# Kernel tuning notes

Measured on AMD Instinct MI355X. Metric: run time of the kernel, lower is better.

Reference implementation:

```python
import jax, jax.numpy as jnp
import numpy as np

K = 4  # knn_graph(k=4, loop=False) hard-coded in H2GCN.forward


def _knn_2hop_adj(Fet, k):
    """Per-batch kNN graph -> symmetrize -> 2-hop binary adjacency [B,N,N].

    Matches create_adj + get_2hop_neighbors: edge direction and the row
    normalization in create_adj are irrelevant because get_2hop_neighbors
    symmetrizes (adj[row,col]=adj[col,row]=1) and thresholds (adj@adj > 0).
    """
    B, N, _ = Fet.shape
    sq = jnp.sum(Fet * Fet, axis=-1)  # [B,N]
    dist = sq[:, :, None] + sq[:, None, :] - 2.0 * jnp.einsum('bnf,bmf->bnm', Fet, Fet)
    eye = jnp.eye(N, dtype=bool)
    dist = jnp.where(eye[None], jnp.inf, dist)  # loop=False: exclude self
    _, idx = jax.lax.top_k(-dist, k)  # [B,N,k] nearest-neighbor indices
    b_idx = jnp.arange(B)[:, None, None]
    n_idx = jnp.arange(N)[None, :, None]
    A = jnp.zeros((B, N, N), Fet.dtype).at[b_idx, n_idx, idx].set(1.0)
    A = jnp.maximum(A, jnp.swapaxes(A, 1, 2))  # symmetrize 1-hop
    A2 = jnp.einsum('bnm,bmk->bnk', A, A)      # 2-hop counts
    A2 = jnp.where(eye[None], 0.0, A2)          # fill_diagonal_(0)
    return (A2 > 0).astype(Fet.dtype)


def _h2gcn_conv(x, A2, w1, b1, w2, b2):
    """H2GCNConv on dense binary adjacency.

    Dense matmul with binary A2 == gather(x[col]) -> fc2 -> index_add over rows;
    A2.sum(-1) == bincount(row). Degree clamped to >= 1.
    """
    ego = jnp.einsum('bnf,of->bno', x, w1) + b1   # fc1(x)
    msg = jnp.einsum('bnf,of->bno', x, w2) + b2   # fc2(x)
    agg = jnp.einsum('bnm,bmo->bno', A2, msg)     # scatter-add of neighbor msgs
    deg = jnp.maximum(jnp.sum(A2, axis=-1, keepdims=True), 1.0)
    return jax.nn.relu(jnp.concatenate([ego, agg / deg], axis=-1))


def setup_inputs() -> dict:
    key = jax.random.key(0)
    ks = jax.random.split(key, 8)
    B, N, F, NH, NC = 128, 197, 768, 512, 1000
    s = 0.02
    return {
        'Fet': jax.random.normal(ks[0], (B, N, F), jnp.float32),
        'w1_0': jax.random.normal(ks[1], (NH, F), jnp.float32) * s,
        'b1_0': jnp.zeros((NH,), jnp.float32),
        'w2_0': jax.random.normal(ks[2], (NH, F), jnp.float32) * s,
        'b2_0': jnp.zeros((NH,), jnp.float32),
        'w1_1': jax.random.normal(ks[3], (NH, 2 * NH), jnp.float32) * s,
        'b1_1': jnp.zeros((NH,), jnp.float32),
        'w2_1': jax.random.normal(ks[4], (NH, 2 * NH), jnp.float32) * s,
        'b2_1': jnp.zeros((NH,), jnp.float32),
        'fc1_w': jax.random.normal(ks[5], (NH, 4 * NH), jnp.float32) * s,
        'fc1_b': jnp.zeros((NH,), jnp.float32),
        'fc2_w': jax.random.normal(ks[6], (NC, NH), jnp.float32) * s,
        'fc2_b': jnp.zeros((NC,), jnp.float32),
    }


def reference(Fet, w1_0, b1_0, w2_0, b2_0, w1_1, b1_1, w2_1, b2_1,
              fc1_w, fc1_b, fc2_w, fc2_b):
    A2 = _knn_2hop_adj(Fet, K)
    h1 = _h2gcn_conv(Fet, A2, w1_0, b1_0, w2_0, b2_0)   # [B,N,2*nhid]
    h2 = _h2gcn_conv(h1, A2, w1_1, b1_1, w2_1, b2_1)    # [B,N,2*nhid]
    h = jnp.concatenate([h1, h2], axis=-1)              # [B,N,final_dim]
    graph_features = jnp.mean(h, axis=1)                # global_mean_pool
    p = jax.nn.relu(graph_features @ fc1_w.T + fc1_b)   # dropout is identity (eval)
    out = p @ fc2_w.T + fc2_b
    return (out, graph_features)
```

## Files before the change

kernel.cpp:

```cpp
#include <hip/hip_runtime.h>
#include <hip/hip_bf16.h>
#include <math.h>

typedef __attribute__((ext_vector_type(8))) short bf16x8;
typedef __attribute__((ext_vector_type(4))) float f32x4;

#define B_ 128
#define N_ 197
#define F_ 768
#define NH_ 512
#define D2_ 1024
#define D4_ 2048
#define NC_ 1000
#define ROWS_ (B_ * N_)
#define KA_ 224
#define NA_ 256

#define OFF_DIST   0ull
#define OFF_SQ     19871232ull
#define OFF_ABITS  19972352ull
#define OFF_DEG    20779520ull
#define OFF_FETHI  20880640ull
#define OFF_MSG    59710720ull
#define OFF_H1     85564672ull
#define OFF_FETLO  OFF_MSG
#define OFF_POOL   137338112ull
#define OFF_P      138386688ull
#define OFF_W10    138648832ull
#define OFF_W20    139435264ull
#define OFF_W11    140221696ull
#define OFF_W21    141270272ull

__device__ __forceinline__ void gll16(const void* g, void* l) {
  __builtin_amdgcn_global_load_lds((const __attribute__((address_space(1))) void*)g,
                                   (__attribute__((address_space(3))) void*)l, 16, 0, 0);
}

__global__ __launch_bounds__(256) void cast_bf16_kernel(const float* __restrict__ src,
                                                        __hip_bfloat16* __restrict__ dst,
                                                        int n4) {
  int i = blockIdx.x * 256 + threadIdx.x;
  if (i >= n4) return;
  float4 v = ((const float4*)src)[i];
  union { __hip_bfloat16 h[4]; uint2 u; } pk;
  pk.h[0] = __float2bfloat16(v.x);
  pk.h[1] = __float2bfloat16(v.y);
  pk.h[2] = __float2bfloat16(v.z);
  pk.h[3] = __float2bfloat16(v.w);
  ((uint2*)dst)[i] = pk.u;
}

__global__ __launch_bounds__(256) void cast_hilo_kernel(const float* __restrict__ src,
                                                        __hip_bfloat16* __restrict__ hi,
                                                        __hip_bfloat16* __restrict__ lo,
                                                        int n4) {
  int i = blockIdx.x * 256 + threadIdx.x;
  if (i >= n4) return;
  float4 v = ((const float4*)src)[i];
  float f[4] = {v.x, v.y, v.z, v.w};
  union { __hip_bfloat16 h[4]; uint2 u; } ph, pl;
#pragma unroll
  for (int k = 0; k < 4; k++) {
    __hip_bfloat16 h = __float2bfloat16(f[k]);
    ph.h[k] = h;
    pl.h[k] = __float2bfloat16(f[k] - __bfloat162float(h));
  }
  ((uint2*)hi)[i] = ph.u;
  ((uint2*)lo)[i] = pl.u;
}

__global__ __launch_bounds__(256) void sqnorm_kernel(const float* __restrict__ X,
                                                     float* __restrict__ sq) {
  int row = blockIdx.x * 4 + (threadIdx.x >> 6);
  int lane = threadIdx.x & 63;
  const float4* xp = (const float4*)(X + (size_t)row * F_);
  float s = 0.f;
#pragma unroll
  for (int i = 0; i < 3; i++) {
    float4 v = xp[lane + i * 64];
    s += v.x * v.x + v.y * v.y + v.z * v.z + v.w * v.w;
  }
#pragma unroll
  for (int o = 32; o > 0; o >>= 1) s += __shfl_down(s, o);
  if (lane == 0) sq[row] = s;
}

__global__ __launch_bounds__(256) void mfma_gram(const __hip_bfloat16* __restrict__ Xhi,
                                                 const __hip_bfloat16* __restrict__ Xlo,
                                                 const float* __restrict__ sq,
                                                 float* __restrict__ dist) {
  __shared__ short AsH[4096];
  __shared__ short BsH[4096];
  __shared__ short AsL[4096];
  __shared__ short BsL[4096];
  const int t = threadIdx.x;
  const int b = blockIdx.z;
  const int bx = blockIdx.x;
  const int m0 = (bx == 0) ? 0 : 128;
  const int o0 = (bx == 2) ? 128 : 0;
  const bool mirror = (bx == 1);
  const int l = t & 63, w = t >> 6;
  const int wm = (w >> 1) * 64, wn = (w & 1) * 64;
  const int frow = l & 15, fch = l >> 4;
  const int srow = t >> 2, sslot = t & 3;
  const size_t rowbase = (size_t)b * N_;
  const char* AhiB = (const char*)(Xhi + (rowbase + m0) * F_);
  const char* AloB = (const char*)(Xlo + (rowbase + m0) * F_);
  const char* BhiB = (const char*)(Xhi + (rowbase + o0) * F_);
  const char* BloB = (const char*)(Xlo + (rowbase + o0) * F_);
  const int rb = F_ * 2;
  char* AsHB = (char*)AsH;
  char* BsHB = (char*)BsH;
  char* AsLB = (char*)AsL;
  char* BsLB = (char*)BsL;
  f32x4 zero = {0.f, 0.f, 0.f, 0.f};
  f32x4 acc[4][4];
#pragma unroll
  for (int i = 0; i < 4; i++)
#pragma unroll
    for (int j = 0; j < 4; j++) acc[i][j] = zero;
  for (int kt = 0; kt < F_ / 32; kt++) {
    const int kb = kt * 64;
#pragma unroll
    for (int u = 0; u < 2; u++) {
      int grow = u * 64 + srow;
      int gslot = sslot ^ (grow & 3);
      size_t go = (size_t)grow * rb + kb + gslot * 16;
      gll16(AhiB + go, AsHB + u * 4096 + t * 16);
      gll16(BhiB + go, BsHB + u * 4096 + t * 16);
      gll16(AloB + go, AsLB + u * 4096 + t * 16);
      gll16(BloB + go, BsLB + u * 4096 + t * 16);
    }
    __syncthreads();
    bf16x8 ah[4], al[4], bh[4], bl[4];
#pragma unroll
    for (int i = 0; i < 4; i++) {
      int ar = wm + i * 16 + frow;
      int aoff = ar * 64 + ((fch ^ (ar & 3)) * 16);
      ah[i] = *(const bf16x8*)(AsHB + aoff);
      al[i] = *(const bf16x8*)(AsLB + aoff);
      int br = wn + i * 16 + frow;
      int boff = br * 64 + ((fch ^ (br & 3)) * 16);
      bh[i] = *(const bf16x8*)(BsHB + boff);
      bl[i] = *(const bf16x8*)(BsLB + boff);
    }
#pragma unroll
    for (int i = 0; i < 4; i++)
#pragma unroll
      for (int j = 0; j < 4; j++) {
        acc[i][j] = __builtin_amdgcn_mfma_f32_16x16x32_bf16(ah[i], bh[j], acc[i][j], 0, 0, 0);
        acc[i][j] = __builtin_amdgcn_mfma_f32_16x16x32_bf16(ah[i], bl[j], acc[i][j], 0, 0, 0);
        acc[i][j] = __builtin_amdgcn_mfma_f32_16x16x32_bf16(al[i], bh[j], acc[i][j], 0, 0, 0);
      }
    __syncthreads();
  }
#pragma unroll
  for (int j = 0; j < 4; j++) {
    int m = o0 + wn + j * 16 + frow;
    if (m >= N_) continue;
    float sm = sq[rowbase + m];
#pragma unroll
    for (int i = 0; i < 4; i++) {
      int nb = m0 + wm + i * 16 + fch * 4;
#pragma unroll
      for (int r = 0; r < 4; r++) {
        int n = nb + r;
        if (n >= N_) continue;
        float d = sq[rowbase + n] + sm - 2.f * acc[i][j][r];
        if (n == m) d = INFINITY;
        dist[(rowbase + n) * N_ + m] = d;
        if (mirror) dist[(rowbase + m) * N_ + n] = d;
      }
    }
  }
}

__global__ __launch_bounds__(256) void topk_kernel(const float* __restrict__ dist,
                                                   unsigned long long* __restrict__ Abits) {
  int row = blockIdx.x * 4 + (threadIdx.x >> 6);
  int lane = threadIdx.x & 63;
  int b = row / N_, n = row - b * N_;
  const float* dr = dist + (size_t)row * N_;
  float v[4];
  int vi[4];
#pragma unroll
  for (int i = 0; i < 4; i++) {
    int m = lane + i * 64;
    bool ok = (m < N_);
    v[i] = ok ? dr[m] : INFINITY;
    vi[i] = ok ? m : 0x3fffffff;
  }
  unsigned long long nbr[4] = {0ull, 0ull, 0ull, 0ull};
#pragma unroll
  for (int t = 0; t < 4; t++) {
    float bv = v[0];
    int bi = vi[0];
#pragma unroll
    for (int i = 1; i < 4; i++)
      if (v[i] < bv || (v[i] == bv && vi[i] < bi)) { bv = v[i]; bi = vi[i]; }
#pragma unroll
    for (int o = 1; o < 64; o <<= 1) {
      float ov = __shfl_xor(bv, o);
      int oi = __shfl_xor(bi, o);
      if (ov < bv || (ov == bv && oi < bi)) { bv = ov; bi = oi; }
    }
#pragma unroll
    for (int i = 0; i < 4; i++)
      if (vi[i] == bi) { v[i] = INFINITY; vi[i] = 0x3fffffff; }
    if (lane == 0) {
      nbr[bi >> 6] |= 1ull << (bi & 63);
      atomicOr(&Abits[((size_t)b * N_ + bi) * 4 + (n >> 6)], 1ull << (n & 63));
    }
  }
  if (lane == 0) {
#pragma unroll
    for (int w = 0; w < 4; w++)
      if (nbr[w]) atomicOr(&Abits[(size_t)row * 4 + w], nbr[w]);
  }
}

__global__ __launch_bounds__(256) void a2_kernel(const unsigned long long* __restrict__ Abits,
                                                 __hip_bfloat16* __restrict__ A2bf,
                                                 float* __restrict__ deg) {
  int row = blockIdx.x * 4 + (threadIdx.x >> 6);
  int lane = threadIdx.x & 63;
  int b = row / N_, n = row - b * N_;
  const unsigned long long* arow = Abits + (size_t)row * 4;
  const unsigned long long* base = Abits + (size_t)b * N_ * 4;
  unsigned long long r0 = 0, r1 = 0, r2 = 0, r3 = 0;
#pragma unroll
  for (int w = 0; w < 4; w++) {
    if ((arow[w] >> lane) & 1ull) {
      const unsigned long long* mr = base + (size_t)(w * 64 + lane) * 4;
      r0 |= mr[0]; r1 |= mr[1]; r2 |= mr[2]; r3 |= mr[3];
    }
  }
#pragma unroll
  for (int o = 1; o < 64; o <<= 1) {
    r0 |= __shfl_xor(r0, o);
    r1 |= __shfl_xor(r1, o);
    r2 |= __shfl_xor(r2, o);
    r3 |= __shfl_xor(r3, o);
  }
  unsigned long long rr[4] = {r0, r1, r2, r3};
  rr[n >> 6] &= ~(1ull << (n & 63));
  __hip_bfloat16* out = A2bf + ((size_t)b * NA_ + n) * KA_;
  const __hip_bfloat16 one = __float2bfloat16(1.f);
  const __hip_bfloat16 zer = __float2bfloat16(0.f);
#pragma unroll
  for (int i = 0; i < 4; i++) {
    int m = lane + i * 64;
    if (m < KA_)
      out[m] = (m < N_ && ((rr[m >> 6] >> (m & 63)) & 1ull)) ? one : zer;
  }
  if (lane == 0) {
    int dg = __popcll(rr[0]) + __popcll(rr[1]) + __popcll(rr[2]) + __popcll(rr[3]);
    deg[row] = (float)(dg > 0 ? dg : 1);
  }
}

template <bool RELU>
__global__ __launch_bounds__(256) void mfma_linear(const __hip_bfloat16* __restrict__ X,
                                                   const __hip_bfloat16* __restrict__ W,
                                                   const float* __restrict__ bias,
                                                   __hip_bfloat16* __restrict__ Y,
                                                   int K, int ldy, int colOff) {
  __shared__ short As[4096];
  __shared__ short Bs[4096];
  const int t = threadIdx.x;
  const int m0 = blockIdx.y * 128, o0 = blockIdx.x * 128;
  const int l = t & 63, w = t >> 6;
  const int wm = (w >> 1) * 64, wn = (w & 1) * 64;
  const int frow = l & 15, fch = l >> 4;
  const int srow = t >> 2, sslot = t & 3;
  const char* Abase = (const char*)(X + (size_t)m0 * K);
  const char* Bbase = (const char*)(W + (size_t)o0 * K);
  const int rb = K * 2;
  char* AsB = (char*)As;
  char* BsB = (char*)Bs;
  f32x4 zero = {0.f, 0.f, 0.f, 0.f};
  f32x4 acc[4][4];
#pragma unroll
  for (int i = 0; i < 4; i++)
#pragma unroll
    for (int j = 0; j < 4; j++) acc[i][j] = zero;
  const int KT = K >> 5;
  for (int kt = 0; kt < KT; kt++) {
    const int kb = kt * 64;
#pragma unroll
    for (int u = 0; u < 2; u++) {
      int grow = u * 64 + srow;
      int gslot = sslot ^ (grow & 3);
      gll16(Abase + (size_t)grow * rb + kb + gslot * 16, AsB + u * 4096 + t * 16);
      gll16(Bbase + (size_t)grow * rb + kb + gslot * 16, BsB + u * 4096 + t * 16);
    }
    __syncthreads();
    bf16x8 af[4], bfv[4];
#pragma unroll
    for (int i = 0; i < 4; i++) {
      int ar = wm + i * 16 + frow;
      af[i] = *(const bf16x8*)(AsB + ar * 64 + ((fch ^ (ar & 3)) * 16));
      int br = wn + i * 16 + frow;
      bfv[i] = *(const bf16x8*)(BsB + br * 64 + ((fch ^ (br & 3)) * 16));
    }
#pragma unroll
    for (int i = 0; i < 4; i++)
#pragma unroll
      for (int j = 0; j < 4; j++)
        acc[i][j] = __builtin_amdgcn_mfma_f32_16x16x32_bf16(af[i], bfv[j], acc[i][j], 0, 0, 0);
    __syncthreads();
  }
#pragma unroll
  for (int j = 0; j < 4; j++) {
    int c = o0 + wn + j * 16 + frow;
    float bv = bias[c];
#pragma unroll
    for (int i = 0; i < 4; i++) {
      int r0 = m0 + wm + i * 16 + fch * 4;
#pragma unroll
      for (int r = 0; r < 4; r++) {
        float v = acc[i][j][r] + bv;
        if (RELU) v = fmaxf(v, 0.f);
        Y[(size_t)(r0 + r) * ldy + colOff + c] = __float2bfloat16(v);
      }
    }
  }
}

__global__ __launch_bounds__(256) void mfma_ego_pool(const __hip_bfloat16* __restrict__ h1,
                                                     const __hip_bfloat16* __restrict__ W,
                                                     const float* __restrict__ bias,
                                                     float* __restrict__ pool, int poolOff) {
  __shared__ short As[4096];
  __shared__ short Bs[4096];
  const int t = threadIdx.x;
  const int b = blockIdx.z;
  const int m0 = blockIdx.y * 128, o0 = blockIdx.x * 128;
  const int l = t & 63, w = t >> 6;
  const int wm = (w >> 1) * 64, wn = (w & 1) * 64;
  const int frow = l & 15, fch = l >> 4;
  const int srow = t >> 2, sslot = t & 3;
  const char* Abase = (const char*)(h1 + ((size_t)b * N_ + m0) * D2_);
  const char* Bbase = (const char*)(W + (size_t)o0 * D2_);
  char* AsB = (char*)As;
  char* BsB = (char*)Bs;
  f32x4 zero = {0.f, 0.f, 0.f, 0.f};
  f32x4 acc[4][4];
#pragma unroll
  for (int i = 0; i < 4; i++)
#pragma unroll
    for (int j = 0; j < 4; j++) acc[i][j] = zero;
  for (int kt = 0; kt < 32; kt++) {
    const int kb = kt * 64;
#pragma unroll
    for (int u = 0; u < 2; u++) {
      int grow = u * 64 + srow;
      int gslot = sslot ^ (grow & 3);
      gll16(Abase + (size_t)grow * (D2_ * 2) + kb + gslot * 16, AsB + u * 4096 + t * 16);
      gll16(Bbase + (size_t)grow * (D2_ * 2) + kb + gslot * 16, BsB + u * 4096 + t * 16);
    }
    __syncthreads();
    bf16x8 af[4], bfv[4];
#pragma unroll
    for (int i = 0; i < 4; i++) {
      int ar = wm + i * 16 + frow;
      af[i] = *(const bf16x8*)(AsB + ar * 64 + ((fch ^ (ar & 3)) * 16));
      int br = wn + i * 16 + frow;
      bfv[i] = *(const bf16x8*)(BsB + br * 64 + ((fch ^ (br & 3)) * 16));
    }
#pragma unroll
    for (int i = 0; i < 4; i++)
#pragma unroll
      for (int j = 0; j < 4; j++)
        acc[i][j] = __builtin_amdgcn_mfma_f32_16x16x32_bf16(af[i], bfv[j], acc[i][j], 0, 0, 0);
    __syncthreads();
  }
#pragma unroll
  for (int j = 0; j < 4; j++) {
    int c = o0 + wn + j * 16 + frow;
    float bv = bias[c];
    float s = 0.f;
#pragma unroll
    for (int i = 0; i < 4; i++) {
#pragma unroll
      for (int r = 0; r < 4; r++) {
        int n = m0 + wm + i * 16 + fch * 4 + r;
        if (n < N_) s += fmaxf(acc[i][j][r] + bv, 0.f);
      }
    }
    s += __shfl_down(s, 32);
    s += __shfl_down(s, 16);
    if (l < 16) atomicAdd(&pool[(size_t)b * D4_ + poolOff + c], s);
  }
}

template <int MODE>
__global__ __launch_bounds__(256) void mfma_agg(const __hip_bfloat16* __restrict__ A2bf,
                                                const __hip_bfloat16* __restrict__ msg,
                                                const float* __restrict__ deg,
                                                __hip_bfloat16* __restrict__ H,
                                                float* __restrict__ pool, int poolOff) {
  __shared__ short As[4096];
  __shared__ short Bs[4096];
  const int t = threadIdx.x;
  const int b = blockIdx.z;
  const int m0 = blockIdx.y * 128, o0 = blockIdx.x * 128;
  const int l = t & 63, w = t >> 6;
  const int wm = (w >> 1) * 64, wn = (w & 1) * 64;
  const int frow = l & 15, fch = l >> 4;
  const int srow = t >> 2, sslot = t & 3;
  const char* Abase = (const char*)(A2bf + ((size_t)b * NA_ + m0) * KA_);
  const __hip_bfloat16* Mb = msg + (size_t)b * N_ * NH_;
  const int bk = t >> 3;
  const int bf0 = (t & 7) * 16;
  char* AsB = (char*)As;
  char* BsB = (char*)Bs;
  f32x4 zero = {0.f, 0.f, 0.f, 0.f};
  f32x4 acc[4][4];
#pragma unroll
  for (int i = 0; i < 4; i++)
#pragma unroll
    for (int j = 0; j < 4; j++) acc[i][j] = zero;
  for (int kt = 0; kt < 7; kt++) {
#pragma unroll
    for (int u = 0; u < 2; u++) {
      int grow = u * 64 + srow;
      int gslot = sslot ^ (grow & 3);
      gll16(Abase + (size_t)grow * (KA_ * 2) + kt * 64 + gslot * 16, AsB + u * 4096 + t * 16);
    }
    int krow = kt * 32 + bk;
    const __hip_bfloat16* mp = Mb + (size_t)krow * NH_ + o0 + bf0;
    bf16x8 v0 = *(const bf16x8*)mp;
    bf16x8 v1 = *(const bf16x8*)(mp + 8);
#pragma unroll
    for (int e = 0; e < 8; e++) {
      int f0a = bf0 + e;
      int f1a = bf0 + 8 + e;
      *(short*)(BsB + f0a * 64 + (((bk >> 3) ^ (f0a & 3)) * 16) + (bk & 7) * 2) = v0[e];
      *(short*)(BsB + f1a * 64 + (((bk >> 3) ^ (f1a & 3)) * 16) + (bk & 7) * 2) = v1[e];
    }
    __syncthreads();
    bf16x8 af[4], bfv[4];
#pragma unroll
    for (int i = 0; i < 4; i++) {
      int ar = wm + i * 16 + frow;
      af[i] = *(const bf16x8*)(AsB + ar * 64 + ((fch ^ (ar & 3)) * 16));
      int br = wn + i * 16 + frow;
      bfv[i] = *(const bf16x8*)(BsB + br * 64 + ((fch ^ (br & 3)) * 16));
    }
#pragma unroll
    for (int i = 0; i < 4; i++)
#pragma unroll
      for (int j = 0; j < 4; j++)
        acc[i][j] = __builtin_amdgcn_mfma_f32_16x16x32_bf16(af[i], bfv[j], acc[i][j], 0, 0, 0);
    __syncthreads();
  }
  if (MODE == 0) {
#pragma unroll
    for (int j = 0; j < 4; j++) {
      int c = o0 + wn + j * 16 + frow;
#pragma unroll
      for (int i = 0; i < 4; i++) {
#pragma unroll
        for (int r = 0; r < 4; r++) {
          int n = m0 + wm + i * 16 + fch * 4 + r;
          if (n < N_) {
            float dv = deg[b * N_ + n];
            float v = fmaxf(acc[i][j][r] / dv, 0.f);
            H[((size_t)b * N_ + n) * D2_ + NH_ + c] = __float2bfloat16(v);
          }
        }
      }
    }
  } else {
#pragma unroll
    for (int j = 0; j < 4; j++) {
      int c = o0 + wn + j * 16 + frow;
      float s = 0.f;
#pragma unroll
      for (int i = 0; i < 4; i++) {
#pragma unroll
        for (int r = 0; r < 4; r++) {
          int n = m0 + wm + i * 16 + fch * 4 + r;
          if (n < N_) {
            float dv = deg[b * N_ + n];
            s += fmaxf(acc[i][j][r] / dv, 0.f);
          }
        }
      }
      s += __shfl_down(s, 32);
      s += __shfl_down(s, 16);
      if (l < 16) atomicAdd(&pool[(size_t)b * D4_ + poolOff + c], s);
    }
  }
}

__global__ __launch_bounds__(256) void pool_kernel(const __hip_bfloat16* __restrict__ h1,
                                                   const float* __restrict__ pool,
                                                   float* __restrict__ gf) {
  int b = blockIdx.y;
  int c = blockIdx.x * 256 + threadIdx.x;
  if (c < D2_) {
    const __hip_bfloat16* p = h1 + (size_t)b * N_ * D2_ + c;
    float s = 0.f;
    for (int n = 0; n < N_; n++) s += __bfloat162float(p[(size_t)n * D2_]);
    gf[(size_t)b * D4_ + c] = s * (1.f / N_);
  } else {
    gf[(size_t)b * D4_ + c] = pool[(size_t)b * D4_ + c] * (1.f / N_);
  }
}

template <bool RELUX>
__global__ __launch_bounds__(256) void head_gemm(const float* __restrict__ Xg,
                                                 const float* __restrict__ W,
                                                 const float* __restrict__ bias,
                                                 float* __restrict__ Y,
                                                 int Rows, int Fin, int O, int kchunk) {
  __shared__ float Xs[16][68];
  __shared__ float Ws[16][68];
  int tx = threadIdx.x, ty = threadIdx.y;
  int tid = ty * 16 + tx;
  int lr = tid >> 2;
  int lk = (tid & 3) * 4;
  int rbase = blockIdx.y * 64;
  int o0 = blockIdx.x * 64;
  int k0base = blockIdx.z * kchunk;
  float acc[4][4] = {};
  for (int k0 = k0base; k0 < k0base + kchunk; k0 += 16) {
    float4 xv = make_float4(0.f, 0.f, 0.f, 0.f);
    if (rbase + lr < Rows) xv = *(const float4*)&Xg[(size_t)(rbase + lr) * Fin + k0 + lk];
    if (RELUX) {
      xv.x = fmaxf(xv.x, 0.f); xv.y = fmaxf(xv.y, 0.f);
      xv.z = fmaxf(xv.z, 0.f); xv.w = fmaxf(xv.w, 0.f);
    }
    Xs[lk][lr] = xv.x; Xs[lk + 1][lr] = xv.y; Xs[lk + 2][lr] = xv.z; Xs[lk + 3][lr] = xv.w;
    float4 wv = make_float4(0.f, 0.f, 0.f, 0.f);
    if (o0 + lr < O) wv = *(const float4*)&W[(size_t)(o0 + lr) * Fin + k0 + lk];
    Ws[lk][lr] = wv.x; Ws[lk + 1][lr] = wv.y; Ws[lk + 2][lr] = wv.z; Ws[lk + 3][lr] = wv.w;
    __syncthreads();
#pragma unroll
    for (int k = 0; k < 16; k++) {
      float4 a = *(const float4*)&Xs[k][ty * 4];
      float4 bb = *(const float4*)&Ws[k][tx * 4];
      float av[4] = {a.x, a.y, a.z, a.w};
      float bv[4] = {bb.x, bb.y, bb.z, bb.w};
#pragma unroll
      for (int i = 0; i < 4; i++)
#pragma unroll
        for (int j = 0; j < 4; j++) acc[i][j] = fmaf(av[i], bv[j], acc[i][j]);
    }
    __syncthreads();
  }
#pragma unroll
  for (int i = 0; i < 4; i++) {
    int rrow = rbase + ty * 4 + i;
    if (rrow >= Rows) continue;
#pragma unroll
    for (int j = 0; j < 4; j++) {
      int c = o0 + tx * 4 + j;
      if (c >= O) continue;
      float vv = acc[i][j] + ((blockIdx.z == 0) ? bias[c] : 0.f);
      atomicAdd(&Y[(size_t)rrow * O + c], vv);
    }
  }
}

extern "C" void kernel_launch(void* const* d_in, const int* in_sizes, int n_in,
                              void* d_out, int out_size, void* d_ws, size_t ws_size,
                              hipStream_t stream) {
  const float* Fet  = (const float*)d_in[0];
  const float* w1_0 = (const float*)d_in[1];
  const float* b1_0 = (const float*)d_in[2];
  const float* w2_0 = (const float*)d_in[3];
  const float* b2_0 = (const float*)d_in[4];
  const float* w1_1 = (const float*)d_in[5];
  const float* b1_1 = (const float*)d_in[6];
  const float* w2_1 = (const float*)d_in[7];
  const float* b2_1 = (const float*)d_in[8];
  const float* fc1_w = (const float*)d_in[9];
  const float* fc1_b = (const float*)d_in[10];
  const float* fc2_w = (const float*)d_in[11];
  const float* fc2_b = (const float*)d_in[12];

  char* ws = (char*)d_ws;
  float* dist = (float*)(ws + OFF_DIST);
  __hip_bfloat16* A2bf = (__hip_bfloat16*)(ws + OFF_DIST);
  float* sq = (float*)(ws + OFF_SQ);
  unsigned long long* Abits = (unsigned long long*)(ws + OFF_ABITS);
  float* deg = (float*)(ws + OFF_DEG);
  __hip_bfloat16* Fet_hi = (__hip_bfloat16*)(ws + OFF_FETHI);
  __hip_bfloat16* Fet_lo = (__hip_bfloat16*)(ws + OFF_FETLO);
  __hip_bfloat16* msg = (__hip_bfloat16*)(ws + OFF_MSG);
  __hip_bfloat16* h1 = (__hip_bfloat16*)(ws + OFF_H1);
  float* pool = (float*)(ws + OFF_POOL);
  float* p = (float*)(ws + OFF_P);
  __hip_bfloat16* w10b = (__hip_bfloat16*)(ws + OFF_W10);
  __hip_bfloat16* w20b = (__hip_bfloat16*)(ws + OFF_W20);
  __hip_bfloat16* w11b = (__hip_bfloat16*)(ws + OFF_W11);
  __hip_bfloat16* w21b = (__hip_bfloat16*)(ws + OFF_W21);

  float* out = (float*)d_out;
  float* gf = out + (size_t)B_ * NC_;

  hipMemsetAsync(Abits, 0, (size_t)ROWS_ * 4 * sizeof(unsigned long long), stream);
  hipMemsetAsync(pool, 0, (size_t)B_ * D4_ * sizeof(float), stream);
  hipMemsetAsync(p, 0, (size_t)B_ * NH_ * sizeof(float), stream);
  hipMemsetAsync(out, 0, (size_t)B_ * NC_ * sizeof(float), stream);

  cast_hilo_kernel<<<(ROWS_ * F_ / 4 + 255) / 256, 256, 0, stream>>>(
      Fet, Fet_hi, Fet_lo, ROWS_ * F_ / 4);
  cast_bf16_kernel<<<384, 256, 0, stream>>>(w1_0, w10b, NH_ * F_ / 4);
  cast_bf16_kernel<<<384, 256, 0, stream>>>(w2_0, w20b, NH_ * F_ / 4);
  cast_bf16_kernel<<<512, 256, 0, stream>>>(w1_1, w11b, NH_ * D2_ / 4);
  cast_bf16_kernel<<<512, 256, 0, stream>>>(w2_1, w21b, NH_ * D2_ / 4);

  sqnorm_kernel<<<ROWS_ / 4, 256, 0, stream>>>(Fet, sq);
  mfma_gram<<<dim3(3, 1, B_), 256, 0, stream>>>(Fet_hi, Fet_lo, sq, dist);
  topk_kernel<<<ROWS_ / 4, 256, 0, stream>>>(dist, Abits);
  a2_kernel<<<ROWS_ / 4, 256, 0, stream>>>(Abits, A2bf, deg);

  mfma_linear<false><<<dim3(4, 197), 256, 0, stream>>>(Fet_hi, w20b, b2_0, msg, F_, NH_, 0);
  mfma_linear<true><<<dim3(4, 197), 256, 0, stream>>>(Fet_hi, w10b, b1_0, h1, F_, D2_, 0);
  mfma_agg<0><<<dim3(4, 2, B_), 256, 0, stream>>>(A2bf, msg, deg, h1, nullptr, 0);

  mfma_linear<false><<<dim3(4, 197), 256, 0, stream>>>(h1, w21b, b2_1, msg, D2_, NH_, 0);
  mfma_ego_pool<<<dim3(4, 2, B_), 256, 0, stream>>>(h1, w11b, b1_1, pool, D2_);
  mfma_agg<1><<<dim3(4, 2, B_), 256, 0, stream>>>(A2bf, msg, deg, nullptr, pool, D2_ + NH_);

  pool_kernel<<<dim3(8, B_), 256, 0, stream>>>(h1, pool, gf);

  head_gemm<false><<<dim3(8, 2, 16), dim3(16, 16), 0, stream>>>(
      gf, fc1_w, fc1_b, p, B_, D4_, NH_, 128);
  head_gemm<true><<<dim3(16, 2, 8), dim3(16, 16), 0, stream>>>(
      p, fc2_w, fc2_b, out, B_, NH_, NC_, 64);
}
```

Baseline: 545.3 us.

## Split-K gram, fuse cast with sqnorm, merge ego/msg linears, pool inside aggregation

The gram kernel is split into two K halves, doubling the block count from 384 to 768, and writes raw partial dot products. The top-k kernel then sums the halves and adds the squared norm, with self excluded by index. The hi/lo cast and the squared-norm pass are fused into one kernel, and the ego and message linears are merged into one GEMM over concatenated weights. The layer-2 ego pooling and layer-1 aggregation pooling now go into the fused epilogues via atomics, dropping mfma_ego_pool and part of pool_kernel. In exchange, the gram step writes an extra full-size buffer and top-k reads two buffers plus sq.

Measured after the change: 535.6 us. About the same (-1.8%).

```diff
diff --git a/kernel.cpp b/kernel.cpp
--- a/kernel.cpp
+++ b/kernel.cpp
@@ -16,7 +16,7 @@
 #define KA_ 224
 #define NA_ 256
 
-#define OFF_DIST   0ull
+#define OFF_DIST0  0ull
 #define OFF_SQ     19871232ull
 #define OFF_ABITS  19972352ull
 #define OFF_DEG    20779520ull
@@ -26,10 +26,9 @@
 #define OFF_FETLO  OFF_MSG
 #define OFF_POOL   137338112ull
 #define OFF_P      138386688ull
-#define OFF_W10    138648832ull
-#define OFF_W20    139435264ull
-#define OFF_W11    140221696ull
-#define OFF_W21    141270272ull
+#define OFF_WC1    138648832ull
+#define OFF_WC2    140221696ull
+#define OFF_DIST1  142318848ull
 
 __device__ __forceinline__ void gll16(const void* g, void* l) {
   __builtin_amdgcn_global_load_lds((const __attribute__((address_space(1))) void*)g,
@@ -50,35 +49,30 @@
   ((uint2*)dst)[i] = pk.u;
 }
 
-__global__ __launch_bounds__(256) void cast_hilo_kernel(const float* __restrict__ src,
-                                                        __hip_bfloat16* __restrict__ hi,
-                                                        __hip_bfloat16* __restrict__ lo,
-                                                        int n4) {
-  int i = blockIdx.x * 256 + threadIdx.x;
-  if (i >= n4) return;
-  float4 v = ((const float4*)src)[i];
-  float f[4] = {v.x, v.y, v.z, v.w};
-  union { __hip_bfloat16 h[4]; uint2 u; } ph, pl;
-#pragma unroll
-  for (int k = 0; k < 4; k++) {
-    __hip_bfloat16 h = __float2bfloat16(f[k]);
-    ph.h[k] = h;
-    pl.h[k] = __float2bfloat16(f[k] - __bfloat162float(h));
-  }
-  ((uint2*)hi)[i] = ph.u;
-  ((uint2*)lo)[i] = pl.u;
-}
-
-__global__ __launch_bounds__(256) void sqnorm_kernel(const float* __restrict__ X,
-                                                     float* __restrict__ sq) {
+__global__ __launch_bounds__(256) void cast_hilo_sq(const float* __restrict__ X,
+                                                    __hip_bfloat16* __restrict__ hi,
+                                                    __hip_bfloat16* __restrict__ lo,
+                                                    float* __restrict__ sq) {
   int row = blockIdx.x * 4 + (threadIdx.x >> 6);
   int lane = threadIdx.x & 63;
   const float4* xp = (const float4*)(X + (size_t)row * F_);
+  uint2* hp = (uint2*)(hi + (size_t)row * F_);
+  uint2* lp = (uint2*)(lo + (size_t)row * F_);
   float s = 0.f;
 #pragma unroll
   for (int i = 0; i < 3; i++) {
     float4 v = xp[lane + i * 64];
     s += v.x * v.x + v.y * v.y + v.z * v.z + v.w * v.w;
+    float f[4] = {v.x, v.y, v.z, v.w};
+    union { __hip_bfloat16 h[4]; uint2 u; } ph, pl;
+#pragma unroll
+    for (int k = 0; k < 4; k++) {
+      __hip_bfloat16 h = __float2bfloat16(f[k]);
+      ph.h[k] = h;
+      pl.h[k] = __float2bfloat16(f[k] - __bfloat162float(h));
+    }
+    hp[lane + i * 64] = ph.u;
+    lp[lane + i * 64] = pl.u;
   }
 #pragma unroll
   for (int o = 32; o > 0; o >>= 1) s += __shfl_down(s, o);
@@ -87,8 +81,8 @@
 
 __global__ __launch_bounds__(256) void mfma_gram(const __hip_bfloat16* __restrict__ Xhi,
                                                  const __hip_bfloat16* __restrict__ Xlo,
-                                                 const float* __restrict__ sq,
-                                                 float* __restrict__ dist) {
+                                                 float* __restrict__ g0,
+                                                 float* __restrict__ g1) {
   __shared__ short AsH[4096];
   __shared__ short BsH[4096];
   __shared__ short AsL[4096];
@@ -96,6 +90,7 @@
   const int t = threadIdx.x;
   const int b = blockIdx.z;
   const int bx = blockIdx.x;
+  const int khalf = blockIdx.y;
   const int m0 = (bx == 0) ? 0 : 128;
   const int o0 = (bx == 2) ? 128 : 0;
   const bool mirror = (bx == 1);
@@ -113,23 +108,25 @@
   char* BsHB = (char*)BsH;
   char* AsLB = (char*)AsL;
   char* BsLB = (char*)BsL;
+  float* go = khalf ? g1 : g0;
   f32x4 zero = {0.f, 0.f, 0.f, 0.f};
   f32x4 acc[4][4];
 #pragma unroll
   for (int i = 0; i < 4; i++)
 #pragma unroll
     for (int j = 0; j < 4; j++) acc[i][j] = zero;
-  for (int kt = 0; kt < F_ / 32; kt++) {
+  const int kt0 = khalf * 12;
+  for (int kt = kt0; kt < kt0 + 12; kt++) {
     const int kb = kt * 64;
 #pragma unroll
     for (int u = 0; u < 2; u++) {
       int grow = u * 64 + srow;
       int gslot = sslot ^ (grow & 3);
-      size_t go = (size_t)grow * rb + kb + gslot * 16;
-      gll16(AhiB + go, AsHB + u * 4096 + t * 16);
-      gll16(BhiB + go, BsHB + u * 4096 + t * 16);
-      gll16(AloB + go, AsLB + u * 4096 + t * 16);
-      gll16(BloB + go, BsLB + u * 4096 + t * 16);
+      size_t goff = (size_t)grow * rb + kb + gslot * 16;
+      gll16(AhiB + goff, AsHB + u * 4096 + t * 16);
+      gll16(BhiB + goff, BsHB + u * 4096 + t * 16);
+      gll16(AloB + goff, AsLB + u * 4096 + t * 16);
+      gll16(BloB + goff, BsLB + u * 4096 + t * 16);
     }
     __syncthreads();
     bf16x8 ah[4], al[4], bh[4], bl[4];
@@ -158,7 +155,6 @@
   for (int j = 0; j < 4; j++) {
     int m = o0 + wn + j * 16 + frow;
     if (m >= N_) continue;
-    float sm = sq[rowbase + m];
 #pragma unroll
     for (int i = 0; i < 4; i++) {
       int nb = m0 + wm + i * 16 + fch * 4;
@@ -166,28 +162,31 @@
       for (int r = 0; r < 4; r++) {
         int n = nb + r;
         if (n >= N_) continue;
-        float d = sq[rowbase + n] + sm - 2.f * acc[i][j][r];
-        if (n == m) d = INFINITY;
-        dist[(rowbase + n) * N_ + m] = d;
-        if (mirror) dist[(rowbase + m) * N_ + n] = d;
+        float g = acc[i][j][r];
+        go[(rowbase + n) * N_ + m] = g;
+        if (mirror) go[(rowbase + m) * N_ + n] = g;
       }
     }
   }
 }
 
-__global__ __launch_bounds__(256) void topk_kernel(const float* __restrict__ dist,
+__global__ __launch_bounds__(256) void topk_kernel(const float* __restrict__ g0,
+                                                   const float* __restrict__ g1,
+                                                   const float* __restrict__ sq,
                                                    unsigned long long* __restrict__ Abits) {
   int row = blockIdx.x * 4 + (threadIdx.x >> 6);
   int lane = threadIdx.x & 63;
   int b = row / N_, n = row - b * N_;
-  const float* dr = dist + (size_t)row * N_;
+  const float* g0r = g0 + (size_t)row * N_;
+  const float* g1r = g1 + (size_t)row * N_;
+  const float* sqb = sq + (size_t)b * N_;
   float v[4];
   int vi[4];
 #pragma unroll
   for (int i = 0; i < 4; i++) {
     int m = lane + i * 64;
-    bool ok = (m < N_);
-    v[i] = ok ? dr[m] : INFINITY;
+    bool ok = (m < N_) && (m != n);
+    v[i] = ok ? (sqb[m] - 2.f * (g0r[m] + g1r[m])) : INFINITY;
     vi[i] = ok ? m : 0x3fffffff;
   }
   unsigned long long nbr[4] = {0ull, 0ull, 0ull, 0ull};
@@ -259,12 +258,15 @@
   }
 }
 
-template <bool RELU>
-__global__ __launch_bounds__(256) void mfma_linear(const __hip_bfloat16* __restrict__ X,
-                                                   const __hip_bfloat16* __restrict__ W,
-                                                   const float* __restrict__ bias,
-                                                   __hip_bfloat16* __restrict__ Y,
-                                                   int K, int ldy, int colOff) {
+template <int MODE>
+__global__ __launch_bounds__(256) void mfma_fused(const __hip_bfloat16* __restrict__ X,
+                                                  const __hip_bfloat16* __restrict__ Wcat,
+                                                  const float* __restrict__ biasE,
+                                                  const float* __restrict__ biasM,
+                                                  __hip_bfloat16* __restrict__ h1,
+                                                  __hip_bfloat16* __restrict__ msg,
+                                                  float* __restrict__ pool,
+                                                  int K) {
   __shared__ short As[4096];
   __shared__ short Bs[4096];
   const int t = threadIdx.x;
@@ -274,7 +276,7 @@
   const int frow = l & 15, fch = l >> 4;
   const int srow = t >> 2, sslot = t & 3;
   const char* Abase = (const char*)(X + (size_t)m0 * K);
-  const char* Bbase = (const char*)(W + (size_t)o0 * K);
+  const char* Bbase = (const char*)(Wcat + (size_t)o0 * K);
   const int rb = K * 2;
   char* AsB = (char*)As;
   char* BsB = (char*)Bs;
@@ -310,87 +312,55 @@
         acc[i][j] = __builtin_amdgcn_mfma_f32_16x16x32_bf16(af[i], bfv[j], acc[i][j], 0, 0, 0);
     __syncthreads();
   }
+  const bool ego = (o0 < 512);
 #pragma unroll
   for (int j = 0; j < 4; j++) {
     int c = o0 + wn + j * 16 + frow;
-    float bv = bias[c];
-#pragma unroll
-    for (int i = 0; i < 4; i++) {
-      int r0 = m0 + wm + i * 16 + fch * 4;
-#pragma unroll
-      for (int r = 0; r < 4; r++) {
-        float v = acc[i][j][r] + bv;
-        if (RELU) v = fmaxf(v, 0.f);
-        Y[(size_t)(r0 + r) * ldy + colOff + c] = __float2bfloat16(v);
+    if (ego) {
+      float bv = biasE[c];
+      if (MODE == 1) {
+#pragma unroll
+        for (int i = 0; i < 4; i++) {
+          int r0 = m0 + wm + i * 16 + fch * 4;
+#pragma unroll
+          for (int r = 0; r < 4; r++) {
+            float v = fmaxf(acc[i][j][r] + bv, 0.f);
+            h1[(size_t)(r0 + r) * D2_ + c] = __float2bfloat16(v);
+          }
+        }
+      } else {
+        int rw = m0 + wm;
+        int b0 = rw / N_;
+        int rB = (b0 + 1) * N_;
+        float sA = 0.f, sB = 0.f;
+#pragma unroll
+        for (int i = 0; i < 4; i++) {
+          int r0 = m0 + wm + i * 16 + fch * 4;
+#pragma unroll
+          for (int r = 0; r < 4; r++) {
+            float v = fmaxf(acc[i][j][r] + bv, 0.f);
+            if (r0 + r < rB) sA += v; else sB += v;
+          }
+        }
+        sA += __shfl_down(sA, 32);
+        sA += __shfl_down(sA, 16);
+        sB += __shfl_down(sB, 32);
+        sB += __shfl_down(sB, 16);
+        if (l < 16) {
+          atomicAdd(&pool[(size_t)b0 * D4_ + D2_ + c], sA);
+          if (rw + 64 > rB) atomicAdd(&pool[(size_t)(b0 + 1) * D4_ + D2_ + c], sB);
+        }
       }
-    }
-  }
-}
-
-__global__ __launch_bounds__(256) void mfma_ego_pool(const __hip_bfloat16* __restrict__ h1,
-                                                     const __hip_bfloat16* __restrict__ W,
-                                                     const float* __restrict__ bias,
-                                                     float* __restrict__ pool, int poolOff) {
-  __shared__ short As[4096];
-  __shared__ short Bs[4096];
-  const int t = threadIdx.x;
-  const int b = blockIdx.z;
-  const int m0 = blockIdx.y * 128, o0 = blockIdx.x * 128;
-  const int l = t & 63, w = t >> 6;
-  const int wm = (w >> 1) * 64, wn = (w & 1) * 64;
-  const int frow = l & 15, fch = l >> 4;
-  const int srow = t >> 2, sslot = t & 3;
-  const char* Abase = (const char*)(h1 + ((size_t)b * N_ + m0) * D2_);
-  const char* Bbase = (const char*)(W + (size_t)o0 * D2_);
-  char* AsB = (char*)As;
-  char* BsB = (char*)Bs;
-  f32x4 zero = {0.f, 0.f, 0.f, 0.f};
-  f32x4 acc[4][4];
-#pragma unroll
-  for (int i = 0; i < 4; i++)
-#pragma unroll
-    for (int j = 0; j < 4; j++) acc[i][j] = zero;
-  for (int kt = 0; kt < 32; kt++) {
-    const int kb = kt * 64;
-#pragma unroll
-    for (int u = 0; u < 2; u++) {
-      int grow = u * 64 + srow;
-      int gslot = sslot ^ (grow & 3);
-      gll16(Abase + (size_t)grow * (D2_ * 2) + kb + gslot * 16, AsB + u * 4096 + t * 16);
-      gll16(Bbase + (size_t)grow * (D2_ * 2) + kb + gslot * 16, BsB + u * 4096 + t * 16);
-    }
-    __syncthreads();
-    bf16x8 af[4], bfv[4];
-#pragma unroll
-    for (int i = 0; i < 4; i++) {
-      int ar = wm + i * 16 + frow;
-      af[i] = *(const bf16x8*)(AsB + ar * 64 + ((fch ^ (ar & 3)) * 16));
-      int br = wn + i * 16 + frow;
-      bfv[i] = *(const bf16x8*)(BsB + br * 64 + ((fch ^ (br & 3)) * 16));
-    }
-#pragma unroll
-    for (int i = 0; i < 4; i++)
-#pragma unroll
-      for (int j = 0; j < 4; j++)
-        acc[i][j] = __builtin_amdgcn_mfma_f32_16x16x32_bf16(af[i], bfv[j], acc[i][j], 0, 0, 0);
-    __syncthreads();
-  }
-#pragma unroll
-  for (int j = 0; j < 4; j++) {
-    int c = o0 + wn + j * 16 + frow;
-    float bv = bias[c];
-    float s = 0.f;
-#pragma unroll
-    for (int i = 0; i < 4; i++) {
-#pragma unroll
-      for (int r = 0; r < 4; r++) {
-        int n = m0 + wm + i * 16 + fch * 4 + r;
-        if (n < N_) s += fmaxf(acc[i][j][r] + bv, 0.f);
+    } else {
+      float bv = biasM[c - 512];
+#pragma unroll
+      for (int i = 0; i < 4; i++) {
+        int r0 = m0 + wm + i * 16 + fch * 4;
+#pragma unroll
+        for (int r = 0; r < 4; r++)
+          msg[(size_t)(r0 + r) * NH_ + (c - 512)] = __float2bfloat16(acc[i][j][r] + bv);
       }
     }
-    s += __shfl_down(s, 32);
-    s += __shfl_down(s, 16);
-    if (l < 16) atomicAdd(&pool[(size_t)b * D4_ + poolOff + c], s);
   }
 }
 
@@ -455,59 +425,45 @@
         acc[i][j] = __builtin_amdgcn_mfma_f32_16x16x32_bf16(af[i], bfv[j], acc[i][j], 0, 0, 0);
     __syncthreads();
   }
-  if (MODE == 0) {
-#pragma unroll
-    for (int j = 0; j < 4; j++) {
-      int c = o0 + wn + j * 16 + frow;
-#pragma unroll
-      for (int i = 0; i < 4; i++) {
-#pragma unroll
-        for (int r = 0; r < 4; r++) {
-          int n = m0 + wm + i * 16 + fch * 4 + r;
-          if (n < N_) {
-            float dv = deg[b * N_ + n];
-            float v = fmaxf(acc[i][j][r] / dv, 0.f);
+#pragma unroll
+  for (int j = 0; j < 4; j++) {
+    int c = o0 + wn + j * 16 + frow;
+    float s = 0.f;
+#pragma unroll
+    for (int i = 0; i < 4; i++) {
+#pragma unroll
+      for (int r = 0; r < 4; r++) {
+        int n = m0 + wm + i * 16 + fch * 4 + r;
+        if (n < N_) {
+          float dv = deg[b * N_ + n];
+          float v = fmaxf(acc[i][j][r] / dv, 0.f);
+          if (MODE == 0)
             H[((size_t)b * N_ + n) * D2_ + NH_ + c] = __float2bfloat16(v);
-          }
+          s += v;
         }
       }
     }
-  } else {
-#pragma unroll
-    for (int j = 0; j < 4; j++) {
-      int c = o0 + wn + j * 16 + frow;
-      float s = 0.f;
-#pragma unroll
-      for (int i = 0; i < 4; i++) {
-#pragma unroll
-        for (int r = 0; r < 4; r++) {
-          int n = m0 + wm + i * 16 + fch * 4 + r;
-          if (n < N_) {
-            float dv = deg[b * N_ + n];
-            s += fmaxf(acc[i][j][r] / dv, 0.f);
-          }
-        }
-      }
-      s += __shfl_down(s, 32);
-      s += __shfl_down(s, 16);
-      if (l < 16) atomicAdd(&pool[(size_t)b * D4_ + poolOff + c], s);
-    }
-  }
-}
-
-__global__ __launch_bounds__(256) void pool_kernel(const __hip_bfloat16* __restrict__ h1,
-                                                   const float* __restrict__ pool,
-                                                   float* __restrict__ gf) {
+    s += __shfl_down(s, 32);
+    s += __shfl_down(s, 16);
+    if (l < 16) atomicAdd(&pool[(size_t)b * D4_ + poolOff + c], s);
+  }
+}
+
+__global__ __launch_bounds__(256) void pool_h1ego(const __hip_bfloat16* __restrict__ h1,
+                                                  float* __restrict__ gf) {
   int b = blockIdx.y;
   int c = blockIdx.x * 256 + threadIdx.x;
-  if (c < D2_) {
-    const __hip_bfloat16* p = h1 + (size_t)b * N_ * D2_ + c;
-    float s = 0.f;
-    for (int n = 0; n < N_; n++) s += __bfloat162float(p[(size_t)n * D2_]);
-    gf[(size_t)b * D4_ + c] = s * (1.f / N_);
-  } else {
-    gf[(size_t)b * D4_ + c] = pool[(size_t)b * D4_ + c] * (1.f / N_);
-  }
+  const __hip_bfloat16* p = h1 + (size_t)b * N_ * D2_ + c;
+  float s = 0.f;
+  for (int n = 0; n < N_; n++) s += __bfloat162float(p[(size_t)n * D2_]);
+  gf[(size_t)b * D4_ + c] = s * (1.f / N_);
+}
+
+__global__ __launch_bounds__(256) void scale_pool(const float* __restrict__ pool,
+                                                  float* __restrict__ gf) {
+  int b = blockIdx.y;
+  int c = NH_ + blockIdx.x * 256 + threadIdx.x;
+  gf[(size_t)b * D4_ + c] = pool[(size_t)b * D4_ + c] * (1.f / N_);
 }
 
 template <bool RELUX>
@@ -583,8 +539,9 @@
   const float* fc2_b = (const float*)d_in[12];
 
   char* ws = (char*)d_ws;
-  float* dist = (float*)(ws + OFF_DIST);
-  __hip_bfloat16* A2bf = (__hip_bfloat16*)(ws + OFF_DIST);
+  float* g0 = (float*)(ws + OFF_DIST0);
+  float* g1 = (float*)(ws + OFF_DIST1);
+  __hip_bfloat16* A2bf = (__hip_bfloat16*)(ws + OFF_DIST0);
   float* sq = (float*)(ws + OFF_SQ);
   unsigned long long* Abits = (unsigned long long*)(ws + OFF_ABITS);
   float* deg = (float*)(ws + OFF_DEG);
@@ -594,10 +551,8 @@
   __hip_bfloat16* h1 = (__hip_bfloat16*)(ws + OFF_H1);
   float* pool = (float*)(ws + OFF_POOL);
   float* p = (float*)(ws + OFF_P);
-  __hip_bfloat16* w10b = (__hip_bfloat16*)(ws + OFF_W10);
-  __hip_bfloat16* w20b = (__hip_bfloat16*)(ws + OFF_W20);
-  __hip_bfloat16* w11b = (__hip_bfloat16*)(ws + OFF_W11);
-  __hip_bfloat16* w21b = (__hip_bfloat16*)(ws + OFF_W21);
+  __hip_bfloat16* wc1 = (__hip_bfloat16*)(ws + OFF_WC1);
+  __hip_bfloat16* wc2 = (__hip_bfloat16*)(ws + OFF_WC2);
 
   float* out = (float*)d_out;
   float* gf = out + (size_t)B_ * NC_;
@@ -607,27 +562,26 @@
   hipMemsetAsync(p, 0, (size_t)B_ * NH_ * sizeof(float), stream);
   hipMemsetAsync(out, 0, (size_t)B_ * NC_ * sizeof(float), stream);
 
-  cast_hilo_kernel<<<(ROWS_ * F_ / 4 + 255) / 256, 256, 0, stream>>>(
-      Fet, Fet_hi, Fet_lo, ROWS_ * F_ / 4);
-  cast_bf16_kernel<<<384, 256, 0, stream>>>(w1_0, w10b, NH_ * F_ / 4);
-  cast_bf16_kernel<<<384, 256, 0, stream>>>(w2_0, w20b, NH_ * F_ / 4);
-  cast_bf16_kernel<<<512, 256, 0, stream>>>(w1_1, w11b, NH_ * D2_ / 4);
-  cast_bf16_kernel<<<512, 256, 0, stream>>>(w2_1, w21b, NH_ * D2_ / 4);
-
-  sqnorm_kernel<<<ROWS_ / 4, 256, 0, stream>>>(Fet, sq);
-  mfma_gram<<<dim3(3, 1, B_), 256, 0, stream>>>(Fet_hi, Fet_lo, sq, dist);
-  topk_kernel<<<ROWS_ / 4, 256, 0, stream>>>(dist, Abits);
+  cast_hilo_sq<<<ROWS_ / 4, 256, 0, stream>>>(Fet, Fet_hi, Fet_lo, sq);
+  cast_bf16_kernel<<<384, 256, 0, stream>>>(w1_0, wc1, NH_ * F_ / 4);
+  cast_bf16_kernel<<<384, 256, 0, stream>>>(w2_0, wc1 + (size_t)NH_ * F_, NH_ * F_ / 4);
+  cast_bf16_kernel<<<512, 256, 0, stream>>>(w1_1, wc2, NH_ * D2_ / 4);
+  cast_bf16_kernel<<<512, 256, 0, stream>>>(w2_1, wc2 + (size_t)NH_ * D2_, NH_ * D2_ / 4);
+
+  mfma_gram<<<dim3(3, 2, B_), 256, 0, stream>>>(Fet_hi, Fet_lo, g0, g1);
+  topk_kernel<<<ROWS_ / 4, 256, 0, stream>>>(g0, g1, sq, Abits);
   a2_kernel<<<ROWS_ / 4, 256, 0, stream>>>(Abits, A2bf, deg);
 
-  mfma_linear<false><<<dim3(4, 197), 256, 0, stream>>>(Fet_hi, w20b, b2_0, msg, F_, NH_, 0);
-  mfma_linear<true><<<dim3(4, 197), 256, 0, stream>>>(Fet_hi, w10b, b1_0, h1, F_, D2_, 0);
-  mfma_agg<0><<<dim3(4, 2, B_), 256, 0, stream>>>(A2bf, msg, deg, h1, nullptr, 0);
-
-  mfma_linear<false><<<dim3(4, 197), 256, 0, stream>>>(h1, w21b, b2_1, msg, D2_, NH_, 0);
-  mfma_ego_pool<<<dim3(4, 2, B_), 256, 0, stream>>>(h1, w11b, b1_1, pool, D2_);
+  mfma_fused<1><<<dim3(8, 197), 256, 0, stream>>>(
+      Fet_hi, wc1, b1_0, b2_0, h1, msg, nullptr, F_);
+  mfma_agg<0><<<dim3(4, 2, B_), 256, 0, stream>>>(A2bf, msg, deg, h1, pool, NH_);
+
+  mfma_fused<2><<<dim3(8, 197), 256, 0, stream>>>(
+      h1, wc2, b1_1, b2_1, nullptr, msg, pool, D2_);
   mfma_agg<1><<<dim3(4, 2, B_), 256, 0, stream>>>(A2bf, msg, deg, nullptr, pool, D2_ + NH_);
 
-  pool_kernel<<<dim3(8, B_), 256, 0, stream>>>(h1, pool, gf);
+  pool_h1ego<<<dim3(2, B_), 256, 0, stream>>>(h1, gf);
+  scale_pool<<<dim3(6, B_), 256, 0, stream>>>(pool, gf);
 
   head_gemm<false><<<dim3(8, 2, 16), dim3(16, 16), 0, stream>>>(
       gf, fc1_w, fc1_b, p, B_, D4_, NH_, 128);
```
